# Kernel optimization log

Measured on AMD Instinct MI355X. Metric: run time of the kernel, lower is better.

Reference implementation:

```python
import jax, jax.numpy as jnp
import numpy as np

B, C, W, H = 1024, 1, 128, 128
NUM_IDS = 64
MARGIN = 0.3


def setup_inputs() -> dict:
    key = jax.random.key(0)
    k1, k2 = jax.random.split(key)
    inputs = jax.random.normal(k1, (B, C, W, H), dtype=jnp.float32)
    targets = jax.random.randint(k2, (B,), 0, NUM_IDS, dtype=jnp.int32)
    return {"inputs": inputs, "targets": targets}


def _dc_align(anchor, other):
    # Batched cross-attention alignment (DCModuleOptimized assumption):
    # modi = softmax(anchor @ other^T / sqrt(h)) @ other, per sample.
    h = anchor.shape[-1]
    scale = 1.0 / jnp.sqrt(jnp.asarray(h, anchor.dtype))
    att = jax.nn.softmax(jnp.einsum('bij,bkj->bik', anchor, other) * scale, axis=-1)
    return jnp.einsum('bik,bkj->bij', att, other)


def reference(inputs, targets):
    b, c, w, h = inputs.shape
    x = inputs.reshape(b, -1)                      # (n, d); requires c == 1 downstream
    n = b
    # Pairwise Euclidean distances, stable clamp as in torch code
    sq = jnp.sum(x * x, axis=1)                    # (n,)
    dist = sq[:, None] + sq[None, :] - 2.0 * (x @ x.T)
    dist = jnp.sqrt(jnp.clip(dist, 1e-12, None))   # (n, n)
    mask = targets[:, None] == targets[None, :]    # (n, n) same-identity mask
    # Vectorized hard mining (replaces the per-row Python loop)
    NEG = jnp.asarray(-1e30, dist.dtype)
    POS = jnp.asarray(1e30, dist.dtype)
    hp_idx = jnp.argmax(jnp.where(mask, dist, NEG), axis=1)   # hardest positive per row
    hn_idx = jnp.argmin(jnp.where(mask, POS, dist), axis=1)   # hardest negative per row
    anchor = x.reshape(b, w, h)
    h_pos = anchor[hp_idx]                         # (b, w, h) gathered hard positives
    h_neg = anchor[hn_idx]                         # (b, w, h) gathered hard negatives
    # DC module applied over the whole batch at once
    modi_pos = _dc_align(anchor, h_pos)
    modi_neg = _dc_align(anchor, h_neg)
    dap = anchor.reshape(b, -1) - modi_pos.reshape(b, -1)
    dan = anchor.reshape(b, -1) - modi_neg.reshape(b, -1)
    dist_ap = jnp.sqrt(jnp.sum(dap * dap, axis=1))
    dist_an = jnp.sqrt(jnp.sum(dan * dan, axis=1))
    # MarginRankingLoss with y = 1: mean(relu(dist_ap - dist_an + margin))
    loss = jnp.mean(jax.nn.relu(dist_ap - dist_an + MARGIN))
    return loss
```

## Files before the change

### kernel.cpp

```cpp
#include <hip/hip_runtime.h>
#include <stdint.h>

#define NSAMP 1024
#define D 16384
#define WH 128
#define MARGIN 0.3f
#define SCALE 0.08838834764831845f
#define RSCALE 11.313708498984761f
#define MARG 0.03f
#define LISTCAP 2048

typedef unsigned int uint;
typedef unsigned short ushort_t;

typedef __attribute__((ext_vector_type(8))) short bf16x8;
typedef __attribute__((ext_vector_type(4))) float f32x4;

__device__ __forceinline__ float bf2f(unsigned short b) {
    return __uint_as_float(((uint)b) << 16);
}
__device__ __forceinline__ unsigned short f2bf(float f) {
    uint u = __float_as_uint(f);
    u += 0x7fffu + ((u >> 16) & 1u);
    return (unsigned short)(u >> 16);
}
__device__ __forceinline__ void gload_lds16(const void* g, void* l) {
    __builtin_amdgcn_global_load_lds(
        (const __attribute__((address_space(1))) uint32_t*)g,
        (__attribute__((address_space(3))) uint32_t*)l, 16, 0, 0);
}
__device__ __forceinline__ int lds_off(int row, int col) {
    return row * 256 + ((((col >> 3) ^ (row & 15)) << 4) | ((col & 7) << 1));
}

__global__ __launch_bounds__(256) void k_norms_hi(const float* __restrict__ x,
                                                  float* __restrict__ sq,
                                                  ushort_t* __restrict__ xhi) {
    int b = blockIdx.x;
    int tid = threadIdx.x;
    const float* xr = x + (size_t)b * D;
    ushort_t* hr = xhi + (size_t)b * D;
    float s = 0.f;
    #pragma unroll
    for (int m = 0; m < 16; ++m) {
        int e = m * 1024 + tid * 4;
        float4 v = *(const float4*)(xr + e);
        s += v.x * v.x + v.y * v.y + v.z * v.z + v.w * v.w;
        ushort4 h;
        h.x = f2bf(v.x); h.y = f2bf(v.y); h.z = f2bf(v.z); h.w = f2bf(v.w);
        *(ushort4*)(hr + e) = h;
    }
    for (int off = 32; off; off >>= 1) s += __shfl_down(s, off, 64);
    __shared__ float red[4];
    if ((tid & 63) == 0) red[tid >> 6] = s;
    __syncthreads();
    if (tid == 0) sq[b] = red[0] + red[1] + red[2] + red[3];
}

__global__ __launch_bounds__(256) void k_gram_hi(const ushort_t* __restrict__ xhi,
                                                 float* __restrict__ Gp, int ksub) {
    int ks = blockIdx.x, bi = blockIdx.y, bj = blockIdx.z;
    int i0 = bi * 128, j0 = bj * 128;
    int tid = threadIdx.x;
    int w = tid >> 6, lane = tid & 63;
    int wm = w & 1, wn = w >> 1;
    int quad = lane >> 4, m16 = lane & 15;
    int srow = lane >> 2, sseg = lane & 3;

    __shared__ __align__(16) ushort_t A_s[2][128 * 32];
    __shared__ __align__(16) ushort_t B_s[2][128 * 32];

    f32x4 acc[4][4];
    #pragma unroll
    for (int ii = 0; ii < 4; ++ii)
        #pragma unroll
        for (int jj = 0; jj < 4; ++jj)
            acc[ii][jj] = (f32x4){0.f, 0.f, 0.f, 0.f};

    const size_t Abase = (size_t)i0 * D;
    const size_t Bbase = (size_t)j0 * D;

    for (int kb = 0; kb < ksub / 64; ++kb) {
        int k0 = ks * ksub + kb * 64;
        #pragma unroll
        for (int kk = 0; kk < 2; ++kk) {
            #pragma unroll
            for (int c = 0; c < 2; ++c) {
                int r = w * 32 + c * 16 + srow;
                size_t go = (size_t)r * D + k0 + kk * 32 + sseg * 8;
                int lo = (w * 32 + c * 16) * 32;
                gload_lds16(xhi + Abase + go, &A_s[kk][lo]);
                gload_lds16(xhi + Bbase + go, &B_s[kk][lo]);
            }
        }
        __syncthreads();

        #pragma unroll
        for (int kk = 0; kk < 2; ++kk) {
            bf16x8 ah[4], bh[4];
            #pragma unroll
            for (int ii = 0; ii < 4; ++ii) {
                int ar = wm * 64 + ii * 16 + m16;
                ah[ii] = *(const bf16x8*)&A_s[kk][ar * 32 + quad * 8];
            }
            #pragma unroll
            for (int jj = 0; jj < 4; ++jj) {
                int br = wn * 64 + jj * 16 + m16;
                bh[jj] = *(const bf16x8*)&B_s[kk][br * 32 + quad * 8];
            }
            #pragma unroll
            for (int ii = 0; ii < 4; ++ii)
                #pragma unroll
                for (int jj = 0; jj < 4; ++jj)
                    acc[ii][jj] = __builtin_amdgcn_mfma_f32_16x16x32_bf16(ah[ii], bh[jj], acc[ii][jj], 0, 0, 0);
        }
        __syncthreads();
    }

    float* Gb = Gp + (size_t)ks * NSAMP * NSAMP;
    #pragma unroll
    for (int ii = 0; ii < 4; ++ii)
        #pragma unroll
        for (int jj = 0; jj < 4; ++jj) {
            int rg = i0 + wm * 64 + ii * 16 + quad * 4;
            int cg = j0 + wn * 64 + jj * 16 + m16;
            #pragma unroll
            for (int r = 0; r < 4; ++r)
                Gb[(size_t)(rg + r) * NSAMP + cg] = acc[ii][jj][r];
        }
}

__global__ __launch_bounds__(256) void k_fold(const float* __restrict__ Gp,
                                              float* __restrict__ G, int nks,
                                              int* __restrict__ cnt) {
    if (blockIdx.x == 0 && threadIdx.x == 0) cnt[0] = 0;
    size_t idx = ((size_t)blockIdx.x * 256 + threadIdx.x) * 4;
    float4 s = *(const float4*)(Gp + idx);
    for (int p = 1; p < nks; ++p) {
        float4 v = *(const float4*)(Gp + (size_t)p * NSAMP * NSAMP + idx);
        s.x += v.x; s.y += v.y; s.z += v.z; s.w += v.w;
    }
    *(float4*)(G + idx) = s;
}

__global__ void k_select_flag(const float* __restrict__ G,
                              const float* __restrict__ sq, const int* __restrict__ tgt,
                              int* __restrict__ hp, int* __restrict__ hn,
                              float* __restrict__ dsq, float* __restrict__ bestd,
                              int* __restrict__ list, int* __restrict__ cnt) {
    int i = blockIdx.x;
    int tid = threadIdx.x;
    float sqi = sq[i];
    int ti = tgt[i];
    float dloc[4]; bool sloc[4];
    float pv = -3.0e38f; int pj = 0x7FFFFFFF;
    float nv = 3.0e38f;  int nj = 0x7FFFFFFF;
    #pragma unroll
    for (int m = 0; m < 4; ++m) {
        int j = tid + 256 * m;
        float g = G[(size_t)i * NSAMP + j];
        float d = sqrtf(fmaxf(sqi + sq[j] - 2.f * g, 1e-12f));
        bool same = (tgt[j] == ti);
        dloc[m] = d; sloc[m] = same;
        float cp = same ? d : -1e30f;
        float cn = same ? 1e30f : d;
        if (cp > pv || (cp == pv && j < pj)) { pv = cp; pj = j; }
        if (cn < nv || (cn == nv && j < nj)) { nv = cn; nj = j; }
    }
    for (int off = 32; off; off >>= 1) {
        float opv = __shfl_down(pv, off, 64); int opj = __shfl_down(pj, off, 64);
        float onv = __shfl_down(nv, off, 64); int onj = __shfl_down(nj, off, 64);
        if (opv > pv || (opv == pv && opj < pj)) { pv = opv; pj = opj; }
        if (onv < nv || (onv == nv && onj < nj)) { nv = onv; nj = onj; }
    }
    __shared__ float spv[4], snv[4];
    __shared__ int spj[4], snj[4];
    __shared__ float bb[2];
    __shared__ int cc[2];
    if ((tid & 63) == 0) { int wv = tid >> 6; spv[wv] = pv; spj[wv] = pj; snv[wv] = nv; snj[wv] = nj; }
    __syncthreads();
    if (tid == 0) {
        for (int wv = 1; wv < 4; ++wv) {
            if (spv[wv] > pv || (spv[wv] == pv && spj[wv] < pj)) { pv = spv[wv]; pj = spj[wv]; }
            if (snv[wv] < nv || (snv[wv] == nv && snj[wv] < nj)) { nv = snv[wv]; nj = snj[wv]; }
        }
        hp[i] = pj; hn[i] = nj;
        dsq[i] = sqi; dsq[NSAMP + i] = sqi;
        bestd[i] = pv; bestd[NSAMP + i] = nv;
        bb[0] = pv; bb[1] = nv;
        cc[0] = 0; cc[1] = 0;
    }
    __syncthreads();
    float bp = bb[0], bn = bb[1];
    int lp = 0, ln = 0;
    #pragma unroll
    for (int m = 0; m < 4; ++m) {
        if (sloc[m] && dloc[m] >= bp - MARG) lp++;
        if (!sloc[m] && dloc[m] <= bn + MARG) ln++;
    }
    if (lp) atomicAdd(&cc[0], lp);
    if (ln) atomicAdd(&cc[1], ln);
    __syncthreads();
    if (tid == 0) {
        if (cc[0] > 1) { int k = atomicAdd(cnt, 1); if (k < LISTCAP) list[k] = i; }
        if (cc[1] > 1) { int k = atomicAdd(cnt, 1); if (k < LISTCAP) list[k] = i | (1 << 16); }
    }
}

__global__ __launch_bounds__(256) void k_fix(const float* __restrict__ G,
                                             const float* __restrict__ sq,
                                             const int* __restrict__ tgt,
                                             const float* __restrict__ x,
                                             const ushort_t* __restrict__ xhi,
                                             const float* __restrict__ bestd,
                                             const int* __restrict__ list,
                                             const int* __restrict__ cnt,
                                             int* __restrict__ hp, int* __restrict__ hn) {
    int n = cnt[0]; if (n > LISTCAP) n = LISTCAP;
    int tid = threadIdx.x;
    __shared__ int cand[32];
    __shared__ int ncand;
    __shared__ float bred[4];
    for (int e = blockIdx.x; e < n; e += gridDim.x) {
        int ent = list[e];
        int i = ent & 0xffff, type = ent >> 16;
        if (tid == 0) ncand = 0;
        __syncthreads();
        float bd = bestd[type * NSAMP + i];
        float sqi = sq[i];
        int ti = tgt[i];
        #pragma unroll
        for (int m = 0; m < 4; ++m) {
            int j = tid + 256 * m;
            float g = G[(size_t)i * NSAMP + j];
            float d = sqrtf(fmaxf(sqi + sq[j] - 2.f * g, 1e-12f));
            bool same = (tgt[j] == ti);
            bool fl = (type == 0) ? (same && d >= bd - MARG)
                                  : (!same && d <= bd + MARG);
            if (fl) { int k = atomicAdd(&ncand, 1); if (k < 32) cand[k] = j; }
        }
        __syncthreads();
        int nc = ncand < 32 ? ncand : 32;
        float bestv = (type == 0) ? -3.0e38f : 3.0e38f;
        int bestj = 0x7FFFFFFF;
        const float* xi = x + (size_t)i * D;
        const ushort_t* hi = xhi + (size_t)i * D;
        for (int c = 0; c < nc; ++c) {
            int j = cand[c];
            const float* xj = x + (size_t)j * D;
            const ushort_t* hj = xhi + (size_t)j * D;
            float corr = 0.f;
            #pragma unroll
            for (int m = 0; m < 16; ++m) {
                int k = m * 1024 + tid * 4;
                float4 xa = *(const float4*)(xi + k);
                float4 xb = *(const float4*)(xj + k);
                ushort4 ha = *(const ushort4*)(hi + k);
                ushort4 hb = *(const ushort4*)(hj + k);
                float a0 = bf2f(ha.x), a1 = bf2f(ha.y), a2 = bf2f(ha.z), a3 = bf2f(ha.w);
                float b0 = bf2f(hb.x), b1 = bf2f(hb.y), b2 = bf2f(hb.z), b3 = bf2f(hb.w);
                corr += a0 * (xb.x - b0) + (xa.x - a0) * b0;
                corr += a1 * (xb.y - b1) + (xa.y - a1) * b1;
                corr += a2 * (xb.z - b2) + (xa.z - a2) * b2;
                corr += a3 * (xb.w - b3) + (xa.w - a3) * b3;
            }
            for (int off = 32; off; off >>= 1) corr += __shfl_down(corr, off, 64);
            if ((tid & 63) == 0) bred[tid >> 6] = corr;
            __syncthreads();
            float cs = bred[0] + bred[1] + bred[2] + bred[3];
            float g = G[(size_t)i * NSAMP + j];
            float d2 = sqi + sq[j] - 2.f * (g + cs);
            float d = sqrtf(fmaxf(d2, 1e-12f));
            if (type == 0) {
                if (d > bestv || (d == bestv && j < bestj)) { bestv = d; bestj = j; }
            } else {
                if (d < bestv || (d == bestv && j < bestj)) { bestv = d; bestj = j; }
            }
            __syncthreads();
        }
        if (tid == 0 && nc > 0) { if (type == 0) hp[i] = bestj; else hn[i] = bestj; }
        __syncthreads();
    }
}

__global__ __launch_bounds__(256) void k_dc_mfma(const ushort_t* __restrict__ xhi,
                                                 const int* __restrict__ hp,
                                                 const int* __restrict__ hn,
                                                 float* __restrict__ dsq) {
    int b = blockIdx.x;
    int which = blockIdx.y;
    int q = blockIdx.z;
    int oidx = (which == 0) ? hp[b] : hn[b];
    const ushort_t* Ag = xhi + (size_t)b * D;
    const ushort_t* Og = xhi + (size_t)oidx * D;

    __shared__ __align__(16) char smem[32768];

    int tid = threadIdx.x;
    int wv = tid >> 6, lane = tid & 63;
    int quad = lane >> 4, m16 = lane & 15;
    int rt = q * 4 + wv;

    bf16x8 af[4];
    #pragma unroll
    for (int ks = 0; ks < 4; ++ks)
        af[ks] = *(const bf16x8*)(Ag + (rt * 16 + m16) * WH + ks * 32 + quad * 8);

    {
        uint4 stg[8];
        #pragma unroll
        for (int k = 0; k < 8; ++k)
            stg[k] = *(const uint4*)((const char*)Og + (size_t)(tid + 256 * k) * 16);
        #pragma unroll
        for (int k = 0; k < 8; ++k) {
            int g = tid + 256 * k;
            *(uint4*)(smem + lds_off(g >> 4, (g & 15) * 8)) = stg[k];
        }
    }
    __syncthreads();

    f32x4 acc[8];
    #pragma unroll
    for (int ti = 0; ti < 8; ++ti)
        acc[ti] = (f32x4){0.f, 0.f, 0.f, 0.f};
    #pragma unroll
    for (int ks = 0; ks < 4; ++ks) {
        bf16x8 of[8];
        #pragma unroll
        for (int ti = 0; ti < 8; ++ti)
            of[ti] = *(const bf16x8*)(smem + lds_off(ti * 16 + m16, (ks * 4 + quad) * 8));
        #pragma unroll
        for (int ti = 0; ti < 8; ++ti)
            acc[ti] = __builtin_amdgcn_mfma_f32_16x16x32_bf16(of[ti], af[ks], acc[ti], 0, 0, 0);
    }

    int c0 = (tid & 31) * 4, h0 = (tid >> 5) * 16;
    uint4 trd[4][2];
    #pragma unroll
    for (int j = 0; j < 4; ++j)
        #pragma unroll
        for (int k = 0; k < 2; ++k)
            trd[j][k] = *(const uint4*)(smem + lds_off(c0 + j, h0 + 8 * k));
    __syncthreads();

    #pragma unroll
    for (int i = 0; i < 16; ++i) {
        uint v[4];
        #pragma unroll
        for (int j = 0; j < 4; ++j) {
            uint wo = ((const uint*)&trd[j][i >> 3])[(i >> 1) & 3];
            v[j] = (i & 1) ? (wo >> 16) : (wo & 0xffffu);
        }
        uint2 pk;
        pk.x = v[0] | (v[1] << 16);
        pk.y = v[2] | (v[3] << 16);
        *(uint2*)(smem + lds_off(h0 + i, c0)) = pk;
    }

    float tpart = 0.f;
    bf16x8 pf[4];
    {
        float mx = -3.0e38f;
        #pragma unroll
        for (int ti = 0; ti < 8; ++ti)
            #pragma unroll
            for (int r = 0; r < 4; ++r) {
                float s = acc[ti][r] * SCALE;
                acc[ti][r] = s;
                mx = fmaxf(mx, s);
            }
        mx = fmaxf(mx, __shfl_xor(mx, 16, 64));
        mx = fmaxf(mx, __shfl_xor(mx, 32, 64));
        float sum = 0.f, tnum = 0.f;
        #pragma unroll
        for (int ti = 0; ti < 8; ++ti)
            #pragma unroll
            for (int r = 0; r < 4; ++r) {
                float s = acc[ti][r];
                float e = __expf(s - mx);
                acc[ti][r] = e;
                sum += e;
                tnum += s * e;
            }
        sum += __shfl_xor(sum, 16, 64);
        sum += __shfl_xor(sum, 32, 64);
        tnum += __shfl_xor(tnum, 16, 64);
        tnum += __shfl_xor(tnum, 32, 64);
        float inv = 1.f / sum;
        tpart = 0.25f * tnum * inv;

        uint Ep[8][2];
        #pragma unroll
        for (int ti = 0; ti < 8; ++ti) {
            Ep[ti][0] = (uint)f2bf(acc[ti][0] * inv) |
                        ((uint)f2bf(acc[ti][1] * inv) << 16);
            Ep[ti][1] = (uint)f2bf(acc[ti][2] * inv) |
                        ((uint)f2bf(acc[ti][3] * inv) << 16);
        }
        int tih = quad >> 1;
        #pragma unroll
        for (int ks = 0; ks < 4; ++ks) {
            union { uint u[4]; bf16x8 v; } fr;
            #pragma unroll
            for (int k = 0; k < 4; ++k) {
                int src = (((quad << 1) + (k >> 1)) & 3) * 16 + m16;
                int a = __shfl((int)Ep[2 * ks + 0][k & 1], src, 64);
                int bsh = __shfl((int)Ep[2 * ks + 1][k & 1], src, 64);
                fr.u[k] = (uint)((tih == 0) ? a : bsh);
            }
            pf[ks] = fr.v;
        }
    }
    __syncthreads();

    #pragma unroll
    for (int tj = 0; tj < 8; ++tj)
        acc[tj] = (f32x4){0.f, 0.f, 0.f, 0.f};
    #pragma unroll
    for (int ks = 0; ks < 4; ++ks) {
        bf16x8 otf[8];
        #pragma unroll
        for (int tj = 0; tj < 8; ++tj)
            otf[tj] = *(const bf16x8*)(smem + lds_off(tj * 16 + m16, (ks * 4 + quad) * 8));
        #pragma unroll
        for (int tj = 0; tj < 8; ++tj)
            acc[tj] = __builtin_amdgcn_mfma_f32_16x16x32_bf16(pf[ks], otf[tj], acc[tj], 0, 0, 0);
    }

    float m2 = 0.f;
    #pragma unroll
    for (int tj = 0; tj < 8; ++tj)
        #pragma unroll
        for (int r = 0; r < 4; ++r) {
            float mvv = acc[tj][r];
            m2 += mvv * mvv;
        }
    float part = m2 - 2.f * RSCALE * tpart;
    for (int off = 32; off; off >>= 1) part += __shfl_down(part, off, 64);
    if (lane == 0) atomicAdd(&dsq[which * NSAMP + b], part);
}

__global__ void k_loss(const float* __restrict__ dsq, float* __restrict__ out) {
    int tid = threadIdx.x;
    float s = 0.f;
    #pragma unroll
    for (int m = 0; m < 4; ++m) {
        int b = tid + 256 * m;
        float ap = sqrtf(fmaxf(dsq[b], 0.f));
        float an = sqrtf(fmaxf(dsq[NSAMP + b], 0.f));
        s += fmaxf(ap - an + MARGIN, 0.f);
    }
    for (int off = 32; off; off >>= 1) s += __shfl_down(s, off, 64);
    __shared__ float red[4];
    if ((tid & 63) == 0) red[tid >> 6] = s;
    __syncthreads();
    if (tid == 0) out[0] = (red[0] + red[1] + red[2] + red[3]) * (1.f / NSAMP);
}

extern "C" void kernel_launch(void* const* d_in, const int* in_sizes, int n_in,
                              void* d_out, int out_size, void* d_ws, size_t ws_size,
                              hipStream_t stream) {
    const float* x = (const float*)d_in[0];
    const int* tgt = (const int*)d_in[1];
    float* out = (float*)d_out;
    char* ws = (char*)d_ws;

    const size_t XB = (size_t)NSAMP * D * 2;
    const size_t GB1 = (size_t)NSAMP * NSAMP * 4;
    int nks = (ws_size >= 16 * GB1 + XB + GB1 + (size_t)65536) ? 16 : 8;

    float* Gp = (float*)ws;
    ushort_t* xhi = (ushort_t*)(ws + nks * GB1);
    float* G = (float*)(ws + nks * GB1 + XB);
    char* tail = ws + nks * GB1 + XB + GB1;
    float* sq = (float*)tail;
    float* dsq = sq + NSAMP;
    float* bestd = dsq + 2 * NSAMP;
    int* hp = (int*)(bestd + 2 * NSAMP);
    int* hn = hp + NSAMP;
    int* list = hn + NSAMP;
    int* cnt = list + LISTCAP;

    k_norms_hi<<<NSAMP, 256, 0, stream>>>(x, sq, xhi);
    k_gram_hi<<<dim3(nks, 8, 8), 256, 0, stream>>>(xhi, Gp, D / nks);
    k_fold<<<NSAMP, 256, 0, stream>>>(Gp, G, nks, cnt);
    k_select_flag<<<NSAMP, 256, 0, stream>>>(G, sq, tgt, hp, hn, dsq, bestd, list, cnt);
    k_fix<<<64, 256, 0, stream>>>(G, sq, tgt, x, xhi, bestd, list, cnt, hp, hn);
    k_dc_mfma<<<dim3(NSAMP, 2, 2), 256, 0, stream>>>(xhi, hp, hn, dsq);
    k_loss<<<1, 256, 0, stream>>>(dsq, out);
}
```

Before: 229.5 us.

## Exploit Gram symmetry: compute upper-triangle tiles with split-K, mirror in fold

The Gram kernel now computes only upper-triangular 128x128 tile pairs. The symmetric lower-grid blocks are repurposed to cover the second half of the K slice for off-diagonal tiles, so redundant MMA work is removed while the grid size stays the same. Partial results go into compact per-tile slots, and a new fold kernel reduces them and writes both the tile and its transpose through shared memory. An XOR swizzle on LDS segment placement is also added to reduce bank conflicts on fragment reads. The trade-off is that diagonal blocks do twice the iterations of off-diagonal ones, which causes load imbalance, and the fold kernel launches far fewer blocks.

```diff
diff --git a/kernel.cpp b/kernel.cpp
--- a/kernel.cpp
+++ b/kernel.cpp
@@ -58,14 +58,23 @@
 }
 
 __global__ __launch_bounds__(256) void k_gram_hi(const ushort_t* __restrict__ xhi,
-                                                 float* __restrict__ Gp, int ksub) {
+                                                 float* __restrict__ Gp,
+                                                 int nks, int ksub) {
     int ks = blockIdx.x, bi = blockIdx.y, bj = blockIdx.z;
-    int i0 = bi * 128, j0 = bj * 128;
+    int ti = bi < bj ? bi : bj;
+    int tj = bi < bj ? bj : bi;
+    bool diag = (bi == bj);
+    int i0 = ti * 128, j0 = tj * 128;
+    int kstart = ks * ksub + ((bi > bj) ? (ksub >> 1) : 0);
+    int niter = diag ? (ksub >> 6) : (ksub >> 7);
+
     int tid = threadIdx.x;
     int w = tid >> 6, lane = tid & 63;
     int wm = w & 1, wn = w >> 1;
     int quad = lane >> 4, m16 = lane & 15;
     int srow = lane >> 2, sseg = lane & 3;
+    int swseg = sseg ^ ((srow >> 1) & 3);
+    int rsw = (quad ^ ((m16 >> 1) & 3)) << 3;
 
     __shared__ __align__(16) ushort_t A_s[2][128 * 32];
     __shared__ __align__(16) ushort_t B_s[2][128 * 32];
@@ -80,14 +89,14 @@
     const size_t Abase = (size_t)i0 * D;
     const size_t Bbase = (size_t)j0 * D;
 
-    for (int kb = 0; kb < ksub / 64; ++kb) {
-        int k0 = ks * ksub + kb * 64;
+    for (int kb = 0; kb < niter; ++kb) {
+        int k0 = kstart + kb * 64;
         #pragma unroll
         for (int kk = 0; kk < 2; ++kk) {
             #pragma unroll
             for (int c = 0; c < 2; ++c) {
                 int r = w * 32 + c * 16 + srow;
-                size_t go = (size_t)r * D + k0 + kk * 32 + sseg * 8;
+                size_t go = (size_t)r * D + k0 + kk * 32 + swseg * 8;
                 int lo = (w * 32 + c * 16) * 32;
                 gload_lds16(xhi + Abase + go, &A_s[kk][lo]);
                 gload_lds16(xhi + Bbase + go, &B_s[kk][lo]);
@@ -101,12 +110,12 @@
             #pragma unroll
             for (int ii = 0; ii < 4; ++ii) {
                 int ar = wm * 64 + ii * 16 + m16;
-                ah[ii] = *(const bf16x8*)&A_s[kk][ar * 32 + quad * 8];
+                ah[ii] = *(const bf16x8*)&A_s[kk][ar * 32 + rsw];
             }
             #pragma unroll
             for (int jj = 0; jj < 4; ++jj) {
                 int br = wn * 64 + jj * 16 + m16;
-                bh[jj] = *(const bf16x8*)&B_s[kk][br * 32 + quad * 8];
+                bh[jj] = *(const bf16x8*)&B_s[kk][br * 32 + rsw];
             }
             #pragma unroll
             for (int ii = 0; ii < 4; ++ii)
@@ -117,30 +126,84 @@
         __syncthreads();
     }
 
-    float* Gb = Gp + (size_t)ks * NSAMP * NSAMP;
+    int slot;
+    if (diag) {
+        slot = bi * nks + ks;
+    } else {
+        int offidx = ti * 7 - (ti * (ti - 1)) / 2 + (tj - ti - 1);
+        slot = 8 * nks + offidx * 2 * nks + 2 * ks + (bi > bj ? 1 : 0);
+    }
+    float* Gb = Gp + ((size_t)slot << 14);
     #pragma unroll
     for (int ii = 0; ii < 4; ++ii)
         #pragma unroll
         for (int jj = 0; jj < 4; ++jj) {
-            int rg = i0 + wm * 64 + ii * 16 + quad * 4;
-            int cg = j0 + wn * 64 + jj * 16 + m16;
+            int rg = wm * 64 + ii * 16 + quad * 4;
+            int cg = wn * 64 + jj * 16 + m16;
             #pragma unroll
             for (int r = 0; r < 4; ++r)
-                Gb[(size_t)(rg + r) * NSAMP + cg] = acc[ii][jj][r];
-        }
-}
-
-__global__ __launch_bounds__(256) void k_fold(const float* __restrict__ Gp,
-                                              float* __restrict__ G, int nks,
-                                              int* __restrict__ cnt) {
-    if (blockIdx.x == 0 && threadIdx.x == 0) cnt[0] = 0;
-    size_t idx = ((size_t)blockIdx.x * 256 + threadIdx.x) * 4;
-    float4 s = *(const float4*)(Gp + idx);
-    for (int p = 1; p < nks; ++p) {
-        float4 v = *(const float4*)(Gp + (size_t)p * NSAMP * NSAMP + idx);
-        s.x += v.x; s.y += v.y; s.z += v.z; s.w += v.w;
-    }
-    *(float4*)(G + idx) = s;
+                Gb[(rg + r) * 128 + cg] = acc[ii][jj][r];
+        }
+}
+
+__global__ __launch_bounds__(256) void k_fold_tri(const float* __restrict__ Gp,
+                                                  float* __restrict__ G, int nks,
+                                                  int* __restrict__ cnt) {
+    if (blockIdx.x == 0 && blockIdx.y == 0 && threadIdx.x == 0) cnt[0] = 0;
+    int t = blockIdx.x;
+    int panel = blockIdx.y;
+    int bi = 0, rem = t;
+    while (rem >= 8 - bi) { rem -= 8 - bi; ++bi; }
+    int bj = bi + rem;
+    bool diag = (bi == bj);
+    int tid = threadIdx.x;
+
+    int base_slot, nsl;
+    if (diag) { base_slot = bi * nks; nsl = nks; }
+    else {
+        int offidx = bi * 7 - (bi * (bi - 1)) / 2 + (bj - bi - 1);
+        base_slot = 8 * nks + offidx * 2 * nks; nsl = 2 * nks;
+    }
+    const float* P = Gp + (((size_t)base_slot) << 14) + panel * 4096;
+
+    float4 s[4];
+    #pragma unroll
+    for (int m = 0; m < 4; ++m)
+        s[m] = *(const float4*)(P + (tid + 256 * m) * 4);
+    for (int p = 1; p < nsl; ++p) {
+        const float* Pp = P + (((size_t)p) << 14);
+        #pragma unroll
+        for (int m = 0; m < 4; ++m) {
+            float4 v = *(const float4*)(Pp + (tid + 256 * m) * 4);
+            s[m].x += v.x; s[m].y += v.y; s[m].z += v.z; s[m].w += v.w;
+        }
+    }
+
+    int i0 = bi * 128, j0 = bj * 128, r0 = panel * 32;
+    __shared__ float ts[32][129];
+    #pragma unroll
+    for (int m = 0; m < 4; ++m) {
+        int p4 = (tid + 256 * m) * 4;
+        int lr = p4 >> 7, lc = p4 & 127;
+        *(float4*)(&G[(size_t)(i0 + r0 + lr) * NSAMP + j0 + lc]) = s[m];
+        if (!diag) {
+            ts[lr][lc] = s[m].x; ts[lr][lc + 1] = s[m].y;
+            ts[lr][lc + 2] = s[m].z; ts[lr][lc + 3] = s[m].w;
+        }
+    }
+    if (diag) return;
+    __syncthreads();
+    int oc = tid >> 1, half = tid & 1;
+    float4 o[4];
+    #pragma unroll
+    for (int k = 0; k < 4; ++k) {
+        int rr = half * 16 + k * 4;
+        o[k].x = ts[rr][oc]; o[k].y = ts[rr + 1][oc];
+        o[k].z = ts[rr + 2][oc]; o[k].w = ts[rr + 3][oc];
+    }
+    float* Gm = &G[(size_t)(j0 + oc) * NSAMP + i0 + r0 + half * 16];
+    #pragma unroll
+    for (int k = 0; k < 4; ++k) *(float4*)(Gm + k * 4) = o[k];
 }
 
 __global__ void k_select_flag(const float* __restrict__ G,
@@ -482,8 +545,8 @@
     int* cnt = list + LISTCAP;
 
     k_norms_hi<<<NSAMP, 256, 0, stream>>>(x, sq, xhi);
-    k_gram_hi<<<dim3(nks, 8, 8), 256, 0, stream>>>(xhi, Gp, D / nks);
-    k_fold<<<NSAMP, 256, 0, stream>>>(Gp, G, nks, cnt);
+    k_gram_hi<<<dim3(nks, 8, 8), 256, 0, stream>>>(xhi, Gp, nks, D / nks);
+    k_fold_tri<<<dim3(36, 4), 256, 0, stream>>>(Gp, G, nks, cnt);
     k_select_flag<<<NSAMP, 256, 0, stream>>>(G, sq, tgt, hp, hn, dsq, bestd, list, cnt);
     k_fix<<<64, 256, 0, stream>>>(G, sq, tgt, x, xhi, bestd, list, cnt, hp, hn);
     k_dc_mfma<<<dim3(NSAMP, 2, 2), 256, 0, stream>>>(xhi, hp, hn, dsq);
```

Result: faster. 221.1 us (-3.7%).
